# Kernel tuning notes

Hardware: AMD Instinct MI355X
Metric: run time of the kernel (lower is better)

Reference implementation:

```python
import jax, jax.numpy as jnp
import numpy as np

B, T, D = 4, 2048, 1024
NUM_HEADS = 16
HEAD_DIM = D // NUM_HEADS
MLP_HIDDEN = int(D * 4.0)  # 4096; gate_proj -> 2*MLP_HIDDEN
LN_EPS = 1e-6
GN_EPS = 1e-5


def rmsnorm(x, eps=1e-8):
    return x * jax.lax.rsqrt(jnp.mean(x * x, axis=-1, keepdims=True) + eps)


def bitlinear(x, w):
    # mmfreelm BitLinear: RMSNorm -> 8-bit per-token act quant (STE) -> ternary weight quant (STE)
    xn = rmsnorm(x)
    s = 127.0 / jnp.clip(jnp.max(jnp.abs(xn), axis=-1, keepdims=True), 1e-5, None)
    xq = xn + jax.lax.stop_gradient(jnp.clip(jnp.round(xn * s), -128, 127) / s - xn)
    ws = 1.0 / jnp.clip(jnp.mean(jnp.abs(w)), 1e-5, None)
    wq = w + jax.lax.stop_gradient(jnp.clip(jnp.round(w * ws), -1, 1) / ws - w)
    return xq @ wq.T


def layernorm(x, eps=LN_EPS):  # non-affine
    mu = jnp.mean(x, axis=-1, keepdims=True)
    var = jnp.mean((x - mu) ** 2, axis=-1, keepdims=True)
    return (x - mu) * jax.lax.rsqrt(var + eps)


def modulate(x, shift, scale):
    return x * (1.0 + scale[:, None, :]) + shift[:, None, :]


def hgrn_attention(x, wi, wf, wg, gnorm_w, wo):
    i = bitlinear(x, wi)
    f = jax.nn.sigmoid(bitlinear(x, wf))
    i = jax.nn.silu(i) * (1.0 - f)  # swiglu(i, 1-f)
    # gated linear recurrence h_t = f_t * h_{t-1} + i_t along time axis
    def combine(c1, c2):
        a1, b1 = c1
        a2, b2 = c2
        return a1 * a2, b1 * a2 + b2
    _, h = jax.lax.associative_scan(combine, (f, i), axis=1)
    g = bitlinear(x, wg)
    hh = h.reshape(B, T, NUM_HEADS, HEAD_DIM)
    gg = g.reshape(B, T, NUM_HEADS, HEAD_DIM)
    # FusedRMSNormSwishGate over head_dim
    o = rmsnorm(hh, GN_EPS) * gnorm_w * (gg * jax.nn.sigmoid(gg))
    return bitlinear(o.reshape(B, T, D), wo)


def hgrn_mlp(x, gate_w, down_w):
    y = bitlinear(x, gate_w)
    gate, y = jnp.split(y, 2, axis=-1)
    return bitlinear(jax.nn.silu(gate) * y, down_w)


def setup_inputs() -> dict:
    key = jax.random.key(0)
    ks = jax.random.split(key, 16)
    p = lambda k, shape: jax.random.normal(k, shape, dtype=jnp.float32) * 0.02
    return {
        "x": jax.random.normal(ks[0], (B, T, D), dtype=jnp.float32),
        "c": jax.random.normal(ks[1], (B, D), dtype=jnp.float32),
        "adaln_w": p(ks[2], (6 * D, D)),
        "adaln_b": jnp.zeros((6 * D,), dtype=jnp.float32),
        "wi": p(ks[3], (D, D)),
        "wf": p(ks[4], (D, D)),
        "wg": p(ks[5], (D, D)),
        "gnorm_w": jnp.ones((HEAD_DIM,), dtype=jnp.float32),
        "wo": p(ks[6], (D, D)),
        "gate_w": p(ks[7], (2 * MLP_HIDDEN, D)),
        "down_w": p(ks[8], (D, MLP_HIDDEN)),
    }


def reference(x, c, adaln_w, adaln_b, wi, wf, wg, gnorm_w, wo, gate_w, down_w):
    params = jax.nn.silu(c) @ adaln_w.T + adaln_b  # [B, 6D]
    (shift_msa, scale_msa, gate_msa,
     shift_mlp, scale_mlp, gate_mlp) = jnp.split(params, 6, axis=1)
    mod_x = modulate(layernorm(x), shift_msa, scale_msa)
    attn_out = hgrn_attention(mod_x, wi, wf, wg, gnorm_w, wo)
    x = x + gate_msa[:, None, :] * attn_out
    mlp_in = modulate(layernorm(x), shift_mlp, scale_mlp)
    x = x + gate_mlp[:, None, :] * hgrn_mlp(mlp_in, gate_w, down_w)
    return x
```

## Files before the change

kernel.cpp:

```cpp
#include <hip/hip_runtime.h>
#include <cstdint>
#include <cstddef>

#define B_   4
#define T_   2048
#define D_   1024
#define NTOK (B_*T_)
#define HID  4096
#define PDIM (6*D_)

typedef int v4i __attribute__((ext_vector_type(4)));

__device__ __forceinline__ float sigf(float x){ return 1.0f/(1.0f+expf(-x)); }

__device__ __forceinline__ float bsum256(float v, float* sm, int tid){
#pragma unroll
  for (int o=32;o;o>>=1) v += __shfl_down(v,o);
  if ((tid&63)==0) sm[tid>>6]=v;
  __syncthreads();
  float r = sm[0]+sm[1]+sm[2]+sm[3];
  __syncthreads();
  return r;
}
__device__ __forceinline__ void bsummax256(float& s, float& m, float* sm, int tid){
#pragma unroll
  for (int o=32;o;o>>=1){ s += __shfl_down(s,o); m = fmaxf(m,__shfl_down(m,o)); }
  if ((tid&63)==0){ sm[tid>>6]=s; sm[4+(tid>>6)]=m; }
  __syncthreads();
  s = sm[0]+sm[1]+sm[2]+sm[3];
  m = fmaxf(fmaxf(sm[4],sm[5]),fmaxf(sm[6],sm[7]));
  __syncthreads();
}

__device__ __forceinline__ uint32_t pack4(float a, float b, float c, float d, float k){
  int q0=(int)rintf(a*k); q0 = q0<-128?-128:(q0>127?127:q0);
  int q1=(int)rintf(b*k); q1 = q1<-128?-128:(q1>127?127:q1);
  int q2=(int)rintf(c*k); q2 = q2<-128?-128:(q2>127?127:q2);
  int q3=(int)rintf(d*k); q3 = q3<-128?-128:(q3>127?127:q3);
  return (uint32_t)(q0&255) | ((uint32_t)(q1&255)<<8) | ((uint32_t)(q2&255)<<16) | ((uint32_t)(q3&255)<<24);
}

struct WMeta {
  const float* w[6];
  int8_t* q[6];
  int n[6];
};

__global__ __launch_bounds__(256) void k_wabs(WMeta meta, float* __restrict__ partial){
  int mat = blockIdx.y;
  const float* w = meta.w[mat];
  int n = meta.n[mat];
  int tid = threadIdx.x;
  float s = 0.f;
  for (int i = blockIdx.x*256 + tid; i < n; i += 256*gridDim.x) s += fabsf(w[i]);
  __shared__ float sm[4];
#pragma unroll
  for (int o=32;o;o>>=1) s += __shfl_down(s,o);
  if ((tid&63)==0) sm[tid>>6]=s;
  __syncthreads();
  if (tid==0) partial[mat*256 + blockIdx.x] = sm[0]+sm[1]+sm[2]+sm[3];
}

__global__ __launch_bounds__(256) void k_wfin(WMeta meta, const float* __restrict__ partial, float* __restrict__ wdeq){
  int mat = blockIdx.x;
  int tid = threadIdx.x;
  float s = partial[mat*256 + tid];
  __shared__ float sm[4];
#pragma unroll
  for (int o=32;o;o>>=1) s += __shfl_down(s,o);
  if ((tid&63)==0) sm[tid>>6]=s;
  __syncthreads();
  if (tid==0){
    float mean = (sm[0]+sm[1]+sm[2]+sm[3]) / (float)meta.n[mat];
    wdeq[mat] = fmaxf(mean, 1e-5f);
  }
}

__global__ __launch_bounds__(256) void k_wquant(WMeta meta, const float* __restrict__ wdeq){
  int mat = blockIdx.y;
  const float* w = meta.w[mat];
  int8_t* q = meta.q[mat];
  int n = meta.n[mat];
  float ws = 1.0f / wdeq[mat];
  for (int i = blockIdx.x*256 + threadIdx.x; i < n; i += 256*gridDim.x){
    int v = (int)rintf(w[i]*ws);
    v = v < -1 ? -1 : (v > 1 ? 1 : v);
    q[i] = (int8_t)v;
  }
}

__global__ __launch_bounds__(256) void k_adaln(const float* __restrict__ c, const float* __restrict__ w,
                                               const float* __restrict__ bias, float* __restrict__ params){
  int wv = threadIdx.x>>6, lane = threadIdx.x&63;
  int oidx = blockIdx.x*4 + wv;
  int b = oidx / PDIM, j = oidx % PDIM;
  const float* cr = c + b*D_;
  const float* wr = w + (size_t)j*D_;
  float s = 0.f;
  for (int k = lane; k < D_; k += 64){
    float cv = cr[k];
    s += (cv*sigf(cv)) * wr[k];
  }
#pragma unroll
  for (int o=32;o;o>>=1) s += __shfl_down(s,o);
  if (lane==0) params[oidx] = s + bias[j];
}

template<int RES>
__global__ __launch_bounds__(256) void k_lnmodq(const float* __restrict__ xin,
    const float* __restrict__ addv, const float* __restrict__ params,
    int shift_off, int scale_off, int gate_off,
    float* __restrict__ x2out, int8_t* __restrict__ xq, float* __restrict__ dq){
  int tok = blockIdx.x;
  int b = tok >> 11;
  int tid = threadIdx.x;
  __shared__ float sm[8];
  const float* pb = params + (size_t)b*PDIM;
  float4 v = ((const float4*)(xin + (size_t)tok*D_))[tid];
  if (RES){
    float4 a = ((const float4*)(addv + (size_t)tok*D_))[tid];
    float4 g = ((const float4*)(pb + gate_off))[tid];
    v.x = fmaf(g.x,a.x,v.x); v.y = fmaf(g.y,a.y,v.y);
    v.z = fmaf(g.z,a.z,v.z); v.w = fmaf(g.w,a.w,v.w);
    ((float4*)(x2out + (size_t)tok*D_))[tid] = v;
  }
  float mu = bsum256(v.x+v.y+v.z+v.w, sm, tid) * (1.0f/D_);
  float t0=v.x-mu, t1=v.y-mu, t2=v.z-mu, t3=v.w-mu;
  float var = bsum256(t0*t0+t1*t1+t2*t2+t3*t3, sm, tid) * (1.0f/D_);
  float rstd = rsqrtf(var + 1e-6f);
  float4 sc = ((const float4*)(pb + scale_off))[tid];
  float4 sh = ((const float4*)(pb + shift_off))[tid];
  float y0 = fmaf(t0*rstd, 1.0f+sc.x, sh.x);
  float y1 = fmaf(t1*rstd, 1.0f+sc.y, sh.y);
  float y2 = fmaf(t2*rstd, 1.0f+sc.z, sh.z);
  float y3 = fmaf(t3*rstd, 1.0f+sc.w, sh.w);
  float ssq = y0*y0+y1*y1+y2*y2+y3*y3;
  float mx = fmaxf(fmaxf(fabsf(y0),fabsf(y1)),fmaxf(fabsf(y2),fabsf(y3)));
  bsummax256(ssq, mx, sm, tid);
  float rms = rsqrtf(ssq*(1.0f/D_) + 1e-8f);
  float a = fmaxf(mx*rms, 1e-5f);
  float s = 127.0f/a;
  float k = rms*s;
  ((uint32_t*)(xq + (size_t)tok*D_))[tid] = pack4(y0,y1,y2,y3,k);
  if (tid==0) dq[tok] = 1.0f/s;
}

template<int FINAL>
__global__ __launch_bounds__(256) void k_gemm(const int8_t* __restrict__ Aq, const int8_t* __restrict__ Bq,
    float* __restrict__ Out, const float* __restrict__ adq, const float* __restrict__ wdq_ptr,
    int N, int K, const float* __restrict__ resid, const float* __restrict__ params){
  __shared__ int8_t lA[8192], lB[8192];
  const int tid = threadIdx.x;
  const int wave = tid>>6, lane = tid&63;
  const int row0 = blockIdx.y<<7, col0 = blockIdx.x<<7;
  const int wm = (wave>>1)<<6, wn = (wave&1)<<6;
  v4i acc[4][4];
#pragma unroll
  for (int m=0;m<4;m++)
#pragma unroll
    for (int n=0;n<4;n++) acc[m][n] = (v4i){0,0,0,0};
  const int rA = lane&15, kg = lane>>4;
  for (int k0=0;k0<K;k0+=64){
#pragma unroll
    for (int p=0;p<2;p++){
      int idx = p*256 + tid;
      int r = idx>>2, cb = (idx&3)<<4;
      const int8_t* ga = Aq + (size_t)(row0+r)*K + k0 + cb;
      const int8_t* gb = Bq + (size_t)(col0+r)*K + k0 + cb;
      __builtin_amdgcn_global_load_lds((const __attribute__((address_space(1))) void*)ga,
        (__attribute__((address_space(3))) void*)(lA + p*4096 + wave*1024), 16, 0, 0);
      __builtin_amdgcn_global_load_lds((const __attribute__((address_space(1))) void*)gb,
        (__attribute__((address_space(3))) void*)(lB + p*4096 + wave*1024), 16, 0, 0);
    }
    __syncthreads();
    const v4i* la4 = (const v4i*)lA;
    const v4i* lb4 = (const v4i*)lB;
    v4i af[4], bf[4];
#pragma unroll
    for (int m=0;m<4;m++) af[m] = la4[((wm + m*16 + rA)<<2) + kg];
#pragma unroll
    for (int n=0;n<4;n++) bf[n] = lb4[((wn + n*16 + rA)<<2) + kg];
#pragma unroll
    for (int m=0;m<4;m++)
#pragma unroll
      for (int n=0;n<4;n++)
        acc[m][n] = __builtin_amdgcn_mfma_i32_16x16x64_i8(af[m], bf[n], acc[m][n], 0, 0, 0);
    __syncthreads();
  }
  float wdq = wdq_ptr[0];
  int rr = (lane>>4)<<2, cl = lane&15;
#pragma unroll
  for (int m=0;m<4;m++){
#pragma unroll
    for (int r=0;r<4;r++){
      int row = row0 + wm + m*16 + rr + r;
      float scale = adq[row]*wdq;
#pragma unroll
      for (int n=0;n<4;n++){
        int col = col0 + wn + n*16 + cl;
        size_t oi = (size_t)row*N + col;
        float val = (float)acc[m][n][r]*scale;
        if (FINAL){
          int bb = row>>11;
          val = resid[oi] + params[(size_t)bb*PDIM + 5*D_ + col]*val;
        }
        Out[oi] = val;
      }
    }
  }
}

__global__ __launch_bounds__(256) void k_gemm_gate(const int8_t* __restrict__ Aq, const int8_t* __restrict__ Wg,
    float* __restrict__ Out, const float* __restrict__ adq, const float* __restrict__ wdq_ptr, int K){
  __shared__ int8_t lA[8192], lBg[8192], lBy[8192];
  const int tid = threadIdx.x;
  const int wave = tid>>6, lane = tid&63;
  const int row0 = blockIdx.y<<7, col0 = blockIdx.x<<7;
  const int wm = (wave>>1)<<6, wn = (wave&1)<<6;
  v4i accg[4][4], accy[4][4];
#pragma unroll
  for (int m=0;m<4;m++)
#pragma unroll
    for (int n=0;n<4;n++){ accg[m][n] = (v4i){0,0,0,0}; accy[m][n] = (v4i){0,0,0,0}; }
  const int rA = lane&15, kg = lane>>4;
  for (int k0=0;k0<K;k0+=64){
#pragma unroll
    for (int p=0;p<2;p++){
      int idx = p*256 + tid;
      int r = idx>>2, cb = (idx&3)<<4;
      const int8_t* ga  = Aq + (size_t)(row0+r)*K + k0 + cb;
      const int8_t* gbg = Wg + (size_t)(col0+r)*K + k0 + cb;
      const int8_t* gby = Wg + (size_t)(HID + col0+r)*K + k0 + cb;
      __builtin_amdgcn_global_load_lds((const __attribute__((address_space(1))) void*)ga,
        (__attribute__((address_space(3))) void*)(lA  + p*4096 + wave*1024), 16, 0, 0);
      __builtin_amdgcn_global_load_lds((const __attribute__((address_space(1))) void*)gbg,
        (__attribute__((address_space(3))) void*)(lBg + p*4096 + wave*1024), 16, 0, 0);
      __builtin_amdgcn_global_load_lds((const __attribute__((address_space(1))) void*)gby,
        (__attribute__((address_space(3))) void*)(lBy + p*4096 + wave*1024), 16, 0, 0);
    }
    __syncthreads();
    const v4i* la4 = (const v4i*)lA;
    const v4i* lg4 = (const v4i*)lBg;
    const v4i* ly4 = (const v4i*)lBy;
    v4i af[4], bg[4], by[4];
#pragma unroll
    for (int m=0;m<4;m++) af[m] = la4[((wm + m*16 + rA)<<2) + kg];
#pragma unroll
    for (int n=0;n<4;n++){ bg[n] = lg4[((wn + n*16 + rA)<<2) + kg]; by[n] = ly4[((wn + n*16 + rA)<<2) + kg]; }
#pragma unroll
    for (int m=0;m<4;m++)
#pragma unroll
      for (int n=0;n<4;n++){
        accg[m][n] = __builtin_amdgcn_mfma_i32_16x16x64_i8(af[m], bg[n], accg[m][n], 0, 0, 0);
        accy[m][n] = __builtin_amdgcn_mfma_i32_16x16x64_i8(af[m], by[n], accy[m][n], 0, 0, 0);
      }
    __syncthreads();
  }
  float wdq = wdq_ptr[0];
  int rr = (lane>>4)<<2, cl = lane&15;
#pragma unroll
  for (int m=0;m<4;m++){
#pragma unroll
    for (int r=0;r<4;r++){
      int row = row0 + wm + m*16 + rr + r;
      float scale = adq[row]*wdq;
#pragma unroll
      for (int n=0;n<4;n++){
        int col = col0 + wn + n*16 + cl;
        float gv = (float)accg[m][n][r]*scale;
        float yv = (float)accy[m][n][r]*scale;
        Out[(size_t)row*HID + col] = gv*sigf(gv)*yv;
      }
    }
  }
}

__global__ __launch_bounds__(256) void k_ewif(float* __restrict__ ibuf, float* __restrict__ fbuf, int n4){
  for (int k = blockIdx.x*256 + threadIdx.x; k < n4; k += gridDim.x*256){
    float4 iv = ((float4*)ibuf)[k];
    float4 fv = ((float4*)fbuf)[k];
    float f0=sigf(fv.x), f1=sigf(fv.y), f2=sigf(fv.z), f3=sigf(fv.w);
    float4 io, fo;
    io.x = iv.x*sigf(iv.x)*(1.0f-f0);
    io.y = iv.y*sigf(iv.y)*(1.0f-f1);
    io.z = iv.z*sigf(iv.z)*(1.0f-f2);
    io.w = iv.w*sigf(iv.w)*(1.0f-f3);
    fo.x=f0; fo.y=f1; fo.z=f2; fo.w=f3;
    ((float4*)ibuf)[k] = io;
    ((float4*)fbuf)[k] = fo;
  }
}

__global__ __launch_bounds__(256) void k_scanA(const float* __restrict__ f, const float* __restrict__ ii,
                                               float* __restrict__ Ac, float* __restrict__ Hc){
  int idx = blockIdx.x*256 + threadIdx.x;
  int ch = idx >> 12;
  int c  = idx & 4095;
  int b = c >> 10, d = c & 1023;
  size_t base = ((size_t)(b*T_ + ch*64))*D_ + d;
  float a = 1.f, h = 0.f;
  for (int t=0;t<64;t++){
    float ft = f[base + (size_t)t*D_];
    float it = ii[base + (size_t)t*D_];
    a *= ft;
    h = ft*h + it;
  }
  Ac[ch*4096 + c] = a;
  Hc[ch*4096 + c] = h;
}
__global__ __launch_bounds__(256) void k_scanB(const float* __restrict__ Ac, const float* __restrict__ Hc,
                                               float* __restrict__ H0){
  int c = blockIdx.x*256 + threadIdx.x;
  float h = 0.f;
  for (int ch=0; ch<32; ch++){
    H0[ch*4096 + c] = h;
    h = Ac[ch*4096 + c]*h + Hc[ch*4096 + c];
  }
}
__global__ __launch_bounds__(256) void k_scanC(const float* __restrict__ f, const float* __restrict__ ii,
                                               const float* __restrict__ H0, float* __restrict__ hout){
  int idx = blockIdx.x*256 + threadIdx.x;
  int ch = idx >> 12;
  int c  = idx & 4095;
  int b = c >> 10, d = c & 1023;
  size_t base = ((size_t)(b*T_ + ch*64))*D_ + d;
  float h = H0[ch*4096 + c];
  for (int t=0;t<64;t++){
    float ft = f[base + (size_t)t*D_];
    float it = ii[base + (size_t)t*D_];
    h = ft*h + it;
    hout[base + (size_t)t*D_] = h;
  }
}

__global__ __launch_bounds__(256) void k_ogateq(const float* __restrict__ h, const float* __restrict__ g,
    const float* __restrict__ gnw, int8_t* __restrict__ xq, float* __restrict__ dq){
  int tok = blockIdx.x, tid = threadIdx.x;
  __shared__ float sm[8];
  float4 hv = ((const float4*)(h + (size_t)tok*D_))[tid];
  float ss = hv.x*hv.x + hv.y*hv.y + hv.z*hv.z + hv.w*hv.w;
  ss += __shfl_xor(ss,1); ss += __shfl_xor(ss,2); ss += __shfl_xor(ss,4); ss += __shfl_xor(ss,8);
  float rh = rsqrtf(ss*(1.0f/64.0f) + 1e-5f);
  float4 gv = ((const float4*)(g + (size_t)tok*D_))[tid];
  int hd = (tid*4)&63;
  float o0 = hv.x*rh*gnw[hd+0]*(gv.x*sigf(gv.x));
  float o1 = hv.y*rh*gnw[hd+1]*(gv.y*sigf(gv.y));
  float o2 = hv.z*rh*gnw[hd+2]*(gv.z*sigf(gv.z));
  float o3 = hv.w*rh*gnw[hd+3]*(gv.w*sigf(gv.w));
  float ssq = o0*o0+o1*o1+o2*o2+o3*o3;
  float mx = fmaxf(fmaxf(fabsf(o0),fabsf(o1)),fmaxf(fabsf(o2),fabsf(o3)));
  bsummax256(ssq, mx, sm, tid);
  float rms = rsqrtf(ssq*(1.0f/D_) + 1e-8f);
  float a = fmaxf(mx*rms, 1e-5f);
  float s = 127.0f/a;
  float k = rms*s;
  ((uint32_t*)(xq + (size_t)tok*D_))[tid] = pack4(o0,o1,o2,o3,k);
  if (tid==0) dq[tok] = 1.0f/s;
}

__global__ __launch_bounds__(256) void k_mlpq(const float* __restrict__ hsw, int8_t* __restrict__ xq,
                                              float* __restrict__ dq){
  int tok = blockIdx.x, tid = threadIdx.x;
  __shared__ float sm[8];
  const float4* r4 = (const float4*)(hsw + (size_t)tok*HID);
  float4 v[4];
  float ssq = 0.f, mx = 0.f;
#pragma unroll
  for (int j=0;j<4;j++){
    v[j] = r4[tid + j*256];
    ssq += v[j].x*v[j].x + v[j].y*v[j].y + v[j].z*v[j].z + v[j].w*v[j].w;
    mx = fmaxf(mx, fmaxf(fmaxf(fabsf(v[j].x),fabsf(v[j].y)),fmaxf(fabsf(v[j].z),fabsf(v[j].w))));
  }
  bsummax256(ssq, mx, sm, tid);
  float rms = rsqrtf(ssq*(1.0f/HID) + 1e-8f);
  float a = fmaxf(mx*rms, 1e-5f);
  float s = 127.0f/a;
  float k = rms*s;
#pragma unroll
  for (int j=0;j<4;j++)
    ((uint32_t*)(xq + (size_t)tok*HID))[tid + j*256] = pack4(v[j].x,v[j].y,v[j].z,v[j].w,k);
  if (tid==0) dq[tok] = 1.0f/s;
}


extern "C" void kernel_launch(void* const* d_in, const int* in_sizes, int n_in,
                              void* d_out, int out_size, void* d_ws, size_t ws_size,
                              hipStream_t stream){
  (void)in_sizes; (void)n_in; (void)out_size; (void)ws_size;
  const float* x     = (const float*)d_in[0];
  const float* c     = (const float*)d_in[1];
  const float* aw    = (const float*)d_in[2];
  const float* ab    = (const float*)d_in[3];
  const float* wi    = (const float*)d_in[4];
  const float* wf    = (const float*)d_in[5];
  const float* wg    = (const float*)d_in[6];
  const float* gnw   = (const float*)d_in[7];
  const float* wo    = (const float*)d_in[8];
  const float* wgate = (const float*)d_in[9];
  const float* wdown = (const float*)d_in[10];
  float* out = (float*)d_out;

  char* ws = (char*)d_ws;
  size_t off = 0;
  auto alloc = [&](size_t b){ size_t r = off; off += (b + 255) & ~(size_t)255; return r; };

  size_t oWQ[6];
  oWQ[0] = alloc(1024*1024);
  oWQ[1] = alloc(1024*1024);
  oWQ[2] = alloc(1024*1024);
  oWQ[3] = alloc(1024*1024);
  oWQ[4] = alloc((size_t)8192*1024);
  oWQ[5] = alloc((size_t)1024*4096);
  size_t oWDEQ = alloc(6*4);
  size_t oPART = alloc(6*256*4);
  size_t oPAR  = alloc((size_t)4*PDIM*4);
  size_t oS1 = alloc(NTOK*4), oS2 = alloc(NTOK*4), oS3 = alloc(NTOK*4), oSH = alloc(NTOK*4);
  size_t oXQA  = alloc((size_t)NTOK*D_);
  size_t oPOOL = alloc((size_t)5*NTOK*D_*4);
  size_t oX2   = alloc((size_t)NTOK*D_*4);
  size_t oSA = alloc((size_t)32*4096*4), oSHc = alloc((size_t)32*4096*4), oSH0 = alloc((size_t)32*4096*4);

  float*  params = (float*)(ws+oPAR);
  float*  wdeq   = (float*)(ws+oWDEQ);
  float*  part   = (float*)(ws+oPART);
  float*  s1 = (float*)(ws+oS1); float* s2 = (float*)(ws+oS2);
  float*  s3 = (float*)(ws+oS3); float* sh = (float*)(ws+oSH);
  int8_t* xqa = (int8_t*)(ws+oXQA);
  float*  bufI  = (float*)(ws+oPOOL);
  float*  bufF  = bufI + (size_t)NTOK*D_;
  float*  bufG  = bufF + (size_t)NTOK*D_;
  float*  bufH  = bufG + (size_t)NTOK*D_;
  float*  bufAT = bufH + (size_t)NTOK*D_;
  float*  hsw   = bufI;
  int8_t* xqh   = (int8_t*)bufAT;
  float*  x2    = (float*)(ws+oX2);
  float*  scAc = (float*)(ws+oSA); float* scHc = (float*)(ws+oSHc); float* scH0 = (float*)(ws+oSH0);

  WMeta meta;
  meta.w[0]=wi; meta.w[1]=wf; meta.w[2]=wg; meta.w[3]=wo; meta.w[4]=wgate; meta.w[5]=wdown;
  for (int m=0;m<6;m++) meta.q[m] = (int8_t*)(ws+oWQ[m]);
  meta.n[0]=meta.n[1]=meta.n[2]=meta.n[3]=1024*1024; meta.n[4]=8192*1024; meta.n[5]=1024*4096;

  k_wabs  <<<dim3(256,6), 256, 0, stream>>>(meta, part);
  k_wfin  <<<6,           256, 0, stream>>>(meta, part, wdeq);
  k_wquant<<<dim3(2048,6),256, 0, stream>>>(meta, wdeq);

  k_adaln<<<PDIM, 256, 0, stream>>>(c, aw, ab, params);

  k_lnmodq<0><<<NTOK, 256, 0, stream>>>(x, nullptr, params, 0, D_, 0, nullptr, xqa, s1);
  k_gemm<0><<<dim3(8,64), 256, 0, stream>>>(xqa, meta.q[0], bufI, s1, wdeq+0, D_, D_, nullptr, nullptr);
  k_gemm<0><<<dim3(8,64), 256, 0, stream>>>(xqa, meta.q[1], bufF, s1, wdeq+1, D_, D_, nullptr, nullptr);
  k_gemm<0><<<dim3(8,64), 256, 0, stream>>>(xqa, meta.q[2], bufG, s1, wdeq+2, D_, D_, nullptr, nullptr);
  k_ewif<<<2048, 256, 0, stream>>>(bufI, bufF, NTOK*D_/4);
  k_scanA<<<512, 256, 0, stream>>>(bufF, bufI, scAc, scHc);
  k_scanB<<<16,  256, 0, stream>>>(scAc, scHc, scH0);
  k_scanC<<<512, 256, 0, stream>>>(bufF, bufI, scH0, bufH);
  k_ogateq<<<NTOK, 256, 0, stream>>>(bufH, bufG, gnw, xqa, s2);
  k_gemm<0><<<dim3(8,64), 256, 0, stream>>>(xqa, meta.q[3], bufAT, s2, wdeq+3, D_, D_, nullptr, nullptr);

  k_lnmodq<1><<<NTOK, 256, 0, stream>>>(x, bufAT, params, 3*D_, 4*D_, 2*D_, x2, xqa, s3);
  k_gemm_gate<<<dim3(32,64), 256, 0, stream>>>(xqa, meta.q[4], hsw, s3, wdeq+4, D_);
  k_mlpq<<<NTOK, 256, 0, stream>>>(hsw, xqh, sh);
  k_gemm<1><<<dim3(8,64), 256, 0, stream>>>(xqh, meta.q[5], out, sh, wdeq+5, D_, HID, x2, params);
}
```

Measured before the change: 703.5 us.

## Double-buffer GEMMs, swizzle LDS, fuse i/f gemms with gating, store bf16 intermediates

Several ideas land together. The int8 GEMMs get double-buffered LDS staging, and an XOR swizzle on the k-word layout is applied when quantizing weights and activations so LDS reads avoid bank conflicts. The wi and wf GEMMs are fused into one kernel whose epilogue applies sigmoid and swiglu, which removes the separate elementwise pass. The i, f, g and MLP hidden intermediates are stored as bf16 instead of fp32 to cut memory traffic. The bf16 storage lowers the precision of values fed into the scan and requantization, and the doubled LDS use may reduce occupancy.

```diff
diff --git a/kernel.cpp b/kernel.cpp
--- a/kernel.cpp
+++ b/kernel.cpp
@@ -10,8 +10,20 @@
 #define PDIM (6*D_)
 
 typedef int v4i __attribute__((ext_vector_type(4)));
+typedef __attribute__((ext_vector_type(8))) unsigned short ushort8v;
 
 __device__ __forceinline__ float sigf(float x){ return 1.0f/(1.0f+expf(-x)); }
+
+__device__ __forceinline__ float b2f(uint16_t u){ union{uint32_t i; float f;} x; x.i = ((uint32_t)u)<<16; return x.f; }
+__device__ __forceinline__ uint16_t f2b(float f){
+  union{float f; uint32_t i;} x; x.f=f;
+  uint32_t r = x.i + 0x7fff + ((x.i>>16)&1);
+  return (uint16_t)(r>>16);
+}
+
+__device__ __forceinline__ int swz_word(int wi, int row){
+  return (wi & ~15) | ((((wi>>2)&3) ^ ((row>>1)&3))<<2) | (wi&3);
+}
 
 __device__ __forceinline__ float bsum256(float v, float* sm, int tid){
 #pragma unroll
@@ -44,6 +56,7 @@
   const float* w[6];
   int8_t* q[6];
   int n[6];
+  int kws[6];
 };
 
 __global__ __launch_bounds__(256) void k_wabs(WMeta meta, float* __restrict__ partial){
@@ -79,13 +92,20 @@
 __global__ __launch_bounds__(256) void k_wquant(WMeta meta, const float* __restrict__ wdeq){
   int mat = blockIdx.y;
   const float* w = meta.w[mat];
-  int8_t* q = meta.q[mat];
-  int n = meta.n[mat];
+  uint32_t* q = (uint32_t*)meta.q[mat];
+  int nw = meta.n[mat]>>2;
+  int kws = meta.kws[mat];
+  int kwmask = (1<<kws)-1;
   float ws = 1.0f / wdeq[mat];
-  for (int i = blockIdx.x*256 + threadIdx.x; i < n; i += 256*gridDim.x){
-    int v = (int)rintf(w[i]*ws);
-    v = v < -1 ? -1 : (v > 1 ? 1 : v);
-    q[i] = (int8_t)v;
+  for (int i = blockIdx.x*256 + threadIdx.x; i < nw; i += 256*gridDim.x){
+    float4 v = ((const float4*)w)[i];
+    int q0=(int)rintf(v.x*ws); q0=q0<-1?-1:(q0>1?1:q0);
+    int q1=(int)rintf(v.y*ws); q1=q1<-1?-1:(q1>1?1:q1);
+    int q2=(int)rintf(v.z*ws); q2=q2<-1?-1:(q2>1?1:q2);
+    int q3=(int)rintf(v.w*ws); q3=q3<-1?-1:(q3>1?1:q3);
+    uint32_t packed = (uint32_t)(q0&255) | ((uint32_t)(q1&255)<<8) | ((uint32_t)(q2&255)<<16) | ((uint32_t)(q3&255)<<24);
+    int row = i >> kws, wi = i & kwmask;
+    q[((size_t)row<<kws) + swz_word(wi,row)] = packed;
   }
 }
 
@@ -141,15 +161,15 @@
   float a = fmaxf(mx*rms, 1e-5f);
   float s = 127.0f/a;
   float k = rms*s;
-  ((uint32_t*)(xq + (size_t)tok*D_))[tid] = pack4(y0,y1,y2,y3,k);
+  ((uint32_t*)(xq + (size_t)tok*D_))[swz_word(tid,tok)] = pack4(y0,y1,y2,y3,k);
   if (tid==0) dq[tok] = 1.0f/s;
 }
 
-template<int FINAL>
+template<int MODE>
 __global__ __launch_bounds__(256) void k_gemm(const int8_t* __restrict__ Aq, const int8_t* __restrict__ Bq,
-    float* __restrict__ Out, const float* __restrict__ adq, const float* __restrict__ wdq_ptr,
+    void* __restrict__ Outv, const float* __restrict__ adq, const float* __restrict__ wdq_ptr,
     int N, int K, const float* __restrict__ resid, const float* __restrict__ params){
-  __shared__ int8_t lA[8192], lB[8192];
+  __shared__ int8_t lA[2][8192], lB[2][8192];
   const int tid = threadIdx.x;
   const int wave = tid>>6, lane = tid&63;
   const int row0 = blockIdx.y<<7, col0 = blockIdx.x<<7;
@@ -160,33 +180,45 @@
 #pragma unroll
     for (int n=0;n<4;n++) acc[m][n] = (v4i){0,0,0,0};
   const int rA = lane&15, kg = lane>>4;
-  for (int k0=0;k0<K;k0+=64){
+  const int axor = (rA>>1)&3;
+  const int r_st = tid>>2, cb_st = (tid&3)<<4;
+
+  auto STAGE = [&](int buf, int k0){
 #pragma unroll
     for (int p=0;p<2;p++){
-      int idx = p*256 + tid;
-      int r = idx>>2, cb = (idx&3)<<4;
-      const int8_t* ga = Aq + (size_t)(row0+r)*K + k0 + cb;
-      const int8_t* gb = Bq + (size_t)(col0+r)*K + k0 + cb;
-      __builtin_amdgcn_global_load_lds((const __attribute__((address_space(1))) void*)ga,
-        (__attribute__((address_space(3))) void*)(lA + p*4096 + wave*1024), 16, 0, 0);
-      __builtin_amdgcn_global_load_lds((const __attribute__((address_space(1))) void*)gb,
-        (__attribute__((address_space(3))) void*)(lB + p*4096 + wave*1024), 16, 0, 0);
+      int r = p*64 + r_st;
+      __builtin_amdgcn_global_load_lds((const __attribute__((address_space(1))) void*)(Aq + (size_t)(row0+r)*K + k0 + cb_st),
+        (__attribute__((address_space(3))) void*)(&lA[buf][p*4096 + wave*1024]), 16, 0, 0);
+      __builtin_amdgcn_global_load_lds((const __attribute__((address_space(1))) void*)(Bq + (size_t)(col0+r)*K + k0 + cb_st),
+        (__attribute__((address_space(3))) void*)(&lB[buf][p*4096 + wave*1024]), 16, 0, 0);
     }
-    __syncthreads();
-    const v4i* la4 = (const v4i*)lA;
-    const v4i* lb4 = (const v4i*)lB;
+  };
+  auto COMPUTE = [&](int buf){
+    const v4i* la4 = (const v4i*)lA[buf];
+    const v4i* lb4 = (const v4i*)lB[buf];
     v4i af[4], bf[4];
 #pragma unroll
-    for (int m=0;m<4;m++) af[m] = la4[((wm + m*16 + rA)<<2) + kg];
-#pragma unroll
-    for (int n=0;n<4;n++) bf[n] = lb4[((wn + n*16 + rA)<<2) + kg];
+    for (int m=0;m<4;m++){ int r = wm + m*16 + rA; af[m] = la4[(r<<2) + (kg^axor)]; }
+#pragma unroll
+    for (int n=0;n<4;n++){ int r = wn + n*16 + rA; bf[n] = lb4[(r<<2) + (kg^axor)]; }
 #pragma unroll
     for (int m=0;m<4;m++)
 #pragma unroll
       for (int n=0;n<4;n++)
         acc[m][n] = __builtin_amdgcn_mfma_i32_16x16x64_i8(af[m], bf[n], acc[m][n], 0, 0, 0);
+  };
+
+  STAGE(0, 0);
+  __syncthreads();
+  int cur = 0;
+  for (int k0=64; k0<K; k0+=64){
+    STAGE(cur^1, k0);
+    COMPUTE(cur);
     __syncthreads();
-  }
+    cur ^= 1;
+  }
+  COMPUTE(cur);
+
   float wdq = wdq_ptr[0];
   int rr = (lane>>4)<<2, cl = lane&15;
 #pragma unroll
@@ -200,98 +232,103 @@
         int col = col0 + wn + n*16 + cl;
         size_t oi = (size_t)row*N + col;
         float val = (float)acc[m][n][r]*scale;
-        if (FINAL){
+        if (MODE==0) ((float*)Outv)[oi] = val;
+        if (MODE==1) ((uint16_t*)Outv)[oi] = f2b(val);
+        if (MODE==2){
           int bb = row>>11;
-          val = resid[oi] + params[(size_t)bb*PDIM + 5*D_ + col]*val;
+          ((float*)Outv)[oi] = resid[oi] + params[(size_t)bb*PDIM + 5*D_ + col]*val;
         }
-        Out[oi] = val;
       }
     }
   }
 }
 
-__global__ __launch_bounds__(256) void k_gemm_gate(const int8_t* __restrict__ Aq, const int8_t* __restrict__ Wg,
-    float* __restrict__ Out, const float* __restrict__ adq, const float* __restrict__ wdq_ptr, int K){
-  __shared__ int8_t lA[8192], lBg[8192], lBy[8192];
+template<int MODE>
+__global__ __launch_bounds__(256) void k_gemm2(const int8_t* __restrict__ Aq, const int8_t* __restrict__ Bq0,
+    const int8_t* __restrict__ Bq1, uint16_t* __restrict__ out0, uint16_t* __restrict__ out1,
+    const float* __restrict__ adq, const float* __restrict__ wdq_ptr, int i0, int i1, int N, int K){
+  __shared__ int8_t lA[2][8192], lB0[2][8192], lB1[2][8192];
   const int tid = threadIdx.x;
   const int wave = tid>>6, lane = tid&63;
   const int row0 = blockIdx.y<<7, col0 = blockIdx.x<<7;
   const int wm = (wave>>1)<<6, wn = (wave&1)<<6;
-  v4i accg[4][4], accy[4][4];
+  v4i acc0[4][4], acc1[4][4];
 #pragma unroll
   for (int m=0;m<4;m++)
 #pragma unroll
-    for (int n=0;n<4;n++){ accg[m][n] = (v4i){0,0,0,0}; accy[m][n] = (v4i){0,0,0,0}; }
+    for (int n=0;n<4;n++){ acc0[m][n] = (v4i){0,0,0,0}; acc1[m][n] = (v4i){0,0,0,0}; }
   const int rA = lane&15, kg = lane>>4;
-  for (int k0=0;k0<K;k0+=64){
+  const int axor = (rA>>1)&3;
+  const int r_st = tid>>2, cb_st = (tid&3)<<4;
+
+  auto STAGE = [&](int buf, int k0){
 #pragma unroll
     for (int p=0;p<2;p++){
-      int idx = p*256 + tid;
-      int r = idx>>2, cb = (idx&3)<<4;
-      const int8_t* ga  = Aq + (size_t)(row0+r)*K + k0 + cb;
-      const int8_t* gbg = Wg + (size_t)(col0+r)*K + k0 + cb;
-      const int8_t* gby = Wg + (size_t)(HID + col0+r)*K + k0 + cb;
-      __builtin_amdgcn_global_load_lds((const __attribute__((address_space(1))) void*)ga,
-        (__attribute__((address_space(3))) void*)(lA  + p*4096 + wave*1024), 16, 0, 0);
-      __builtin_amdgcn_global_load_lds((const __attribute__((address_space(1))) void*)gbg,
-        (__attribute__((address_space(3))) void*)(lBg + p*4096 + wave*1024), 16, 0, 0);
-      __builtin_amdgcn_global_load_lds((const __attribute__((address_space(1))) void*)gby,
-        (__attribute__((address_space(3))) void*)(lBy + p*4096 + wave*1024), 16, 0, 0);
+      int r = p*64 + r_st;
+      __builtin_amdgcn_global_load_lds((const __attribute__((address_space(1))) void*)(Aq  + (size_t)(row0+r)*K + k0 + cb_st),
+        (__attribute__((address_space(3))) void*)(&lA[buf][p*4096 + wave*1024]), 16, 0, 0);
+      __builtin_amdgcn_global_load_lds((const __attribute__((address_space(1))) void*)(Bq0 + (size_t)(col0+r)*K + k0 + cb_st),
+        (__attribute__((address_space(3))) void*)(&lB0[buf][p*4096 + wave*1024]), 16, 0, 0);
+      __builtin_amdgcn_global_load_lds((const __attribute__((address_space(1))) void*)(Bq1 + (size_t)(col0+r)*K + k0 + cb_st),
+        (__attribute__((address_space(3))) void*)(&lB1[buf][p*4096 + wave*1024]), 16, 0, 0);
     }
+  };
+  auto COMPUTE = [&](int buf){
+    const v4i* la4 = (const v4i*)lA[buf];
+    const v4i* lb4 = (const v4i*)lB0[buf];
+    const v4i* lc4 = (const v4i*)lB1[buf];
+    v4i af[4], bf[4], cf[4];
+#pragma unroll
+    for (int m=0;m<4;m++){ int r = wm + m*16 + rA; af[m] = la4[(r<<2) + (kg^axor)]; }
+#pragma unroll
+    for (int n=0;n<4;n++){ int r = wn + n*16 + rA; bf[n] = lb4[(r<<2) + (kg^axor)]; cf[n] = lc4[(r<<2) + (kg^axor)]; }
+#pragma unroll
+    for (int m=0;m<4;m++)
+#pragma unroll
+      for (int n=0;n<4;n++){
+        acc0[m][n] = __builtin_amdgcn_mfma_i32_16x16x64_i8(af[m], bf[n], acc0[m][n], 0, 0, 0);
+        acc1[m][n] = __builtin_amdgcn_mfma_i32_16x16x64_i8(af[m], cf[n], acc1[m][n], 0, 0, 0);
+      }
+  };
+
+  STAGE(0, 0);
+  __syncthreads();
+  int cur = 0;
+  for (int k0=64; k0<K; k0+=64){
+    STAGE(cur^1, k0);
+    COMPUTE(cur);
     __syncthreads();
-    const v4i* la4 = (const v4i*)lA;
-    const v4i* lg4 = (const v4i*)lBg;
-    const v4i* ly4 = (const v4i*)lBy;
-    v4i af[4], bg[4], by[4];
-#pragma unroll
-    for (int m=0;m<4;m++) af[m] = la4[((wm + m*16 + rA)<<2) + kg];
-#pragma unroll
-    for (int n=0;n<4;n++){ bg[n] = lg4[((wn + n*16 + rA)<<2) + kg]; by[n] = ly4[((wn + n*16 + rA)<<2) + kg]; }
-#pragma unroll
-    for (int m=0;m<4;m++)
-#pragma unroll
-      for (int n=0;n<4;n++){
-        accg[m][n] = __builtin_amdgcn_mfma_i32_16x16x64_i8(af[m], bg[n], accg[m][n], 0, 0, 0);
-        accy[m][n] = __builtin_amdgcn_mfma_i32_16x16x64_i8(af[m], by[n], accy[m][n], 0, 0, 0);
-      }
-    __syncthreads();
-  }
-  float wdq = wdq_ptr[0];
+    cur ^= 1;
+  }
+  COMPUTE(cur);
+
+  float wdq0 = wdq_ptr[i0], wdq1 = wdq_ptr[i1];
   int rr = (lane>>4)<<2, cl = lane&15;
 #pragma unroll
   for (int m=0;m<4;m++){
 #pragma unroll
     for (int r=0;r<4;r++){
       int row = row0 + wm + m*16 + rr + r;
-      float scale = adq[row]*wdq;
+      float scale = adq[row];
 #pragma unroll
       for (int n=0;n<4;n++){
         int col = col0 + wn + n*16 + cl;
-        float gv = (float)accg[m][n][r]*scale;
-        float yv = (float)accy[m][n][r]*scale;
-        Out[(size_t)row*HID + col] = gv*sigf(gv)*yv;
+        size_t oi = (size_t)row*N + col;
+        float v0 = (float)acc0[m][n][r]*scale*wdq0;
+        float v1 = (float)acc1[m][n][r]*scale*wdq1;
+        if (MODE==0){
+          float fs = sigf(v1);
+          out0[oi] = f2b(v0*sigf(v0)*(1.0f-fs));
+          out1[oi] = f2b(fs);
+        } else {
+          out0[oi] = f2b(v0*sigf(v0)*v1);
+        }
       }
     }
   }
 }
 
-__global__ __launch_bounds__(256) void k_ewif(float* __restrict__ ibuf, float* __restrict__ fbuf, int n4){
-  for (int k = blockIdx.x*256 + threadIdx.x; k < n4; k += gridDim.x*256){
-    float4 iv = ((float4*)ibuf)[k];
-    float4 fv = ((float4*)fbuf)[k];
-    float f0=sigf(fv.x), f1=sigf(fv.y), f2=sigf(fv.z), f3=sigf(fv.w);
-    float4 io, fo;
-    io.x = iv.x*sigf(iv.x)*(1.0f-f0);
-    io.y = iv.y*sigf(iv.y)*(1.0f-f1);
-    io.z = iv.z*sigf(iv.z)*(1.0f-f2);
-    io.w = iv.w*sigf(iv.w)*(1.0f-f3);
-    fo.x=f0; fo.y=f1; fo.z=f2; fo.w=f3;
-    ((float4*)ibuf)[k] = io;
-    ((float4*)fbuf)[k] = fo;
-  }
-}
-
-__global__ __launch_bounds__(256) void k_scanA(const float* __restrict__ f, const float* __restrict__ ii,
+__global__ __launch_bounds__(256) void k_scanA(const uint16_t* __restrict__ f, const uint16_t* __restrict__ ii,
                                                float* __restrict__ Ac, float* __restrict__ Hc){
   int idx = blockIdx.x*256 + threadIdx.x;
   int ch = idx >> 12;
@@ -300,8 +337,8 @@
   size_t base = ((size_t)(b*T_ + ch*64))*D_ + d;
   float a = 1.f, h = 0.f;
   for (int t=0;t<64;t++){
-    float ft = f[base + (size_t)t*D_];
-    float it = ii[base + (size_t)t*D_];
+    float ft = b2f(f[base + (size_t)t*D_]);
+    float it = b2f(ii[base + (size_t)t*D_]);
     a *= ft;
     h = ft*h + it;
   }
@@ -317,7 +354,7 @@
     h = Ac[ch*4096 + c]*h + Hc[ch*4096 + c];
   }
 }
-__global__ __launch_bounds__(256) void k_scanC(const float* __restrict__ f, const float* __restrict__ ii,
+__global__ __launch_bounds__(256) void k_scanC(const uint16_t* __restrict__ f, const uint16_t* __restrict__ ii,
                                                const float* __restrict__ H0, float* __restrict__ hout){
   int idx = blockIdx.x*256 + threadIdx.x;
   int ch = idx >> 12;
@@ -326,14 +363,14 @@
   size_t base = ((size_t)(b*T_ + ch*64))*D_ + d;
   float h = H0[ch*4096 + c];
   for (int t=0;t<64;t++){
-    float ft = f[base + (size_t)t*D_];
-    float it = ii[base + (size_t)t*D_];
+    float ft = b2f(f[base + (size_t)t*D_]);
+    float it = b2f(ii[base + (size_t)t*D_]);
     h = ft*h + it;
     hout[base + (size_t)t*D_] = h;
   }
 }
 
-__global__ __launch_bounds__(256) void k_ogateq(const float* __restrict__ h, const float* __restrict__ g,
+__global__ __launch_bounds__(256) void k_ogateq(const float* __restrict__ h, const uint16_t* __restrict__ g,
     const float* __restrict__ gnw, int8_t* __restrict__ xq, float* __restrict__ dq){
   int tok = blockIdx.x, tid = threadIdx.x;
   __shared__ float sm[8];
@@ -341,12 +378,13 @@
   float ss = hv.x*hv.x + hv.y*hv.y + hv.z*hv.z + hv.w*hv.w;
   ss += __shfl_xor(ss,1); ss += __shfl_xor(ss,2); ss += __shfl_xor(ss,4); ss += __shfl_xor(ss,8);
   float rh = rsqrtf(ss*(1.0f/64.0f) + 1e-5f);
-  float4 gv = ((const float4*)(g + (size_t)tok*D_))[tid];
+  ushort4 gv = ((const ushort4*)(g + (size_t)tok*D_))[tid];
+  float g0=b2f(gv.x), g1=b2f(gv.y), g2=b2f(gv.z), g3=b2f(gv.w);
   int hd = (tid*4)&63;
-  float o0 = hv.x*rh*gnw[hd+0]*(gv.x*sigf(gv.x));
-  float o1 = hv.y*rh*gnw[hd+1]*(gv.y*sigf(gv.y));
-  float o2 = hv.z*rh*gnw[hd+2]*(gv.z*sigf(gv.z));
-  float o3 = hv.w*rh*gnw[hd+3]*(gv.w*sigf(gv.w));
+  float o0 = hv.x*rh*gnw[hd+0]*(g0*sigf(g0));
+  float o1 = hv.y*rh*gnw[hd+1]*(g1*sigf(g1));
+  float o2 = hv.z*rh*gnw[hd+2]*(g2*sigf(g2));
+  float o3 = hv.w*rh*gnw[hd+3]*(g3*sigf(g3));
   float ssq = o0*o0+o1*o1+o2*o2+o3*o3;
   float mx = fmaxf(fmaxf(fabsf(o0),fabsf(o1)),fmaxf(fabsf(o2),fabsf(o3)));
   bsummax256(ssq, mx, sm, tid);
@@ -354,31 +392,40 @@
   float a = fmaxf(mx*rms, 1e-5f);
   float s = 127.0f/a;
   float k = rms*s;
-  ((uint32_t*)(xq + (size_t)tok*D_))[tid] = pack4(o0,o1,o2,o3,k);
+  ((uint32_t*)(xq + (size_t)tok*D_))[swz_word(tid,tok)] = pack4(o0,o1,o2,o3,k);
   if (tid==0) dq[tok] = 1.0f/s;
 }
 
-__global__ __launch_bounds__(256) void k_mlpq(const float* __restrict__ hsw, int8_t* __restrict__ xq,
+__global__ __launch_bounds__(256) void k_mlpq(const uint16_t* __restrict__ hsw, int8_t* __restrict__ xq,
                                               float* __restrict__ dq){
   int tok = blockIdx.x, tid = threadIdx.x;
   __shared__ float sm[8];
-  const float4* r4 = (const float4*)(hsw + (size_t)tok*HID);
-  float4 v[4];
+  const ushort8v* r8 = (const ushort8v*)(hsw + (size_t)tok*HID);
+  float v[2][8];
   float ssq = 0.f, mx = 0.f;
 #pragma unroll
-  for (int j=0;j<4;j++){
-    v[j] = r4[tid + j*256];
-    ssq += v[j].x*v[j].x + v[j].y*v[j].y + v[j].z*v[j].z + v[j].w*v[j].w;
-    mx = fmaxf(mx, fmaxf(fmaxf(fabsf(v[j].x),fabsf(v[j].y)),fmaxf(fabsf(v[j].z),fabsf(v[j].w))));
+  for (int j=0;j<2;j++){
+    ushort8v u = r8[tid + j*256];
+#pragma unroll
+    for (int e=0;e<8;e++){
+      float fv = b2f(u[e]);
+      v[j][e] = fv;
+      ssq += fv*fv;
+      mx = fmaxf(mx, fabsf(fv));
+    }
   }
   bsummax256(ssq, mx, sm, tid);
   float rms = rsqrtf(ssq*(1.0f/HID) + 1e-8f);
   float a = fmaxf(mx*rms, 1e-5f);
   float s = 127.0f/a;
   float k = rms*s;
-#pragma unroll
-  for (int j=0;j<4;j++)
-    ((uint32_t*)(xq + (size_t)tok*HID))[tid + j*256] = pack4(v[j].x,v[j].y,v[j].z,v[j].w,k);
+  uint32_t* qw = (uint32_t*)(xq + (size_t)tok*HID);
+#pragma unroll
+  for (int j=0;j<2;j++){
+    int u = tid + j*256;
+    qw[swz_word(2*u,   tok)] = pack4(v[j][0],v[j][1],v[j][2],v[j][3],k);
+    qw[swz_word(2*u+1, tok)] = pack4(v[j][4],v[j][5],v[j][6],v[j][7],k);
+  }
   if (tid==0) dq[tok] = 1.0f/s;
 }
 
@@ -416,7 +463,7 @@
   size_t oPAR  = alloc((size_t)4*PDIM*4);
   size_t oS1 = alloc(NTOK*4), oS2 = alloc(NTOK*4), oS3 = alloc(NTOK*4), oSH = alloc(NTOK*4);
   size_t oXQA  = alloc((size_t)NTOK*D_);
-  size_t oPOOL = alloc((size_t)5*NTOK*D_*4);
+  size_t oPOOL = alloc((size_t)3*NTOK*D_*2 + (size_t)2*NTOK*D_*4);
   size_t oX2   = alloc((size_t)NTOK*D_*4);
   size_t oSA = alloc((size_t)32*4096*4), oSHc = alloc((size_t)32*4096*4), oSH0 = alloc((size_t)32*4096*4);
 
@@ -426,13 +473,13 @@
   float*  s1 = (float*)(ws+oS1); float* s2 = (float*)(ws+oS2);
   float*  s3 = (float*)(ws+oS3); float* sh = (float*)(ws+oSH);
   int8_t* xqa = (int8_t*)(ws+oXQA);
-  float*  bufI  = (float*)(ws+oPOOL);
-  float*  bufF  = bufI + (size_t)NTOK*D_;
-  float*  bufG  = bufF + (size_t)NTOK*D_;
-  float*  bufH  = bufG + (size_t)NTOK*D_;
-  float*  bufAT = bufH + (size_t)NTOK*D_;
-  float*  hsw   = bufI;
-  int8_t* xqh   = (int8_t*)bufAT;
+  uint16_t* bI  = (uint16_t*)(ws+oPOOL);
+  uint16_t* bF  = bI + (size_t)NTOK*D_;
+  uint16_t* bG  = bF + (size_t)NTOK*D_;
+  float*    bufH  = (float*)(bG + (size_t)NTOK*D_);
+  float*    bufAT = bufH + (size_t)NTOK*D_;
+  uint16_t* hsw   = bI;
+  int8_t*   xqh   = (int8_t*)bufAT;
   float*  x2    = (float*)(ws+oX2);
   float*  scAc = (float*)(ws+oSA); float* scHc = (float*)(ws+oSHc); float* scH0 = (float*)(ws+oSH0);
 
@@ -440,26 +487,25 @@
   meta.w[0]=wi; meta.w[1]=wf; meta.w[2]=wg; meta.w[3]=wo; meta.w[4]=wgate; meta.w[5]=wdown;
   for (int m=0;m<6;m++) meta.q[m] = (int8_t*)(ws+oWQ[m]);
   meta.n[0]=meta.n[1]=meta.n[2]=meta.n[3]=1024*1024; meta.n[4]=8192*1024; meta.n[5]=1024*4096;
+  meta.kws[0]=meta.kws[1]=meta.kws[2]=meta.kws[3]=meta.kws[4]=8; meta.kws[5]=10;
 
   k_wabs  <<<dim3(256,6), 256, 0, stream>>>(meta, part);
   k_wfin  <<<6,           256, 0, stream>>>(meta, part, wdeq);
-  k_wquant<<<dim3(2048,6),256, 0, stream>>>(meta, wdeq);
+  k_wquant<<<dim3(1024,6),256, 0, stream>>>(meta, wdeq);
 
   k_adaln<<<PDIM, 256, 0, stream>>>(c, aw, ab, params);
 
   k_lnmodq<0><<<NTOK, 256, 0, stream>>>(x, nullptr, params, 0, D_, 0, nullptr, xqa, s1);
-  k_gemm<0><<<dim3(8,64), 256, 0, stream>>>(xqa, meta.q[0], bufI, s1, wdeq+0, D_, D_, nullptr, nullptr);
-  k_gemm<0><<<dim3(8,64), 256, 0, stream>>>(xqa, meta.q[1], bufF, s1, wdeq+1, D_, D_, nullptr, nullptr);
-  k_gemm<0><<<dim3(8,64), 256, 0, stream>>>(xqa, meta.q[2], bufG, s1, wdeq+2, D_, D_, nullptr, nullptr);
-  k_ewif<<<2048, 256, 0, stream>>>(bufI, bufF, NTOK*D_/4);
-  k_scanA<<<512, 256, 0, stream>>>(bufF, bufI, scAc, scHc);
+  k_gemm2<0><<<dim3(8,64), 256, 0, stream>>>(xqa, meta.q[0], meta.q[1], bI, bF, s1, wdeq, 0, 1, D_, D_);
+  k_gemm<1><<<dim3(8,64), 256, 0, stream>>>(xqa, meta.q[2], bG, s1, wdeq+2, D_, D_, nullptr, nullptr);
+  k_scanA<<<512, 256, 0, stream>>>(bF, bI, scAc, scHc);
   k_scanB<<<16,  256, 0, stream>>>(scAc, scHc, scH0);
-  k_scanC<<<512, 256, 0, stream>>>(bufF, bufI, scH0, bufH);
-  k_ogateq<<<NTOK, 256, 0, stream>>>(bufH, bufG, gnw, xqa, s2);
+  k_scanC<<<512, 256, 0, stream>>>(bF, bI, scH0, bufH);
+  k_ogateq<<<NTOK, 256, 0, stream>>>(bufH, bG, gnw, xqa, s2);
   k_gemm<0><<<dim3(8,64), 256, 0, stream>>>(xqa, meta.q[3], bufAT, s2, wdeq+3, D_, D_, nullptr, nullptr);
 
   k_lnmodq<1><<<NTOK, 256, 0, stream>>>(x, bufAT, params, 3*D_, 4*D_, 2*D_, x2, xqa, s3);
-  k_gemm_gate<<<dim3(32,64), 256, 0, stream>>>(xqa, meta.q[4], hsw, s3, wdeq+4, D_);
+  k_gemm2<1><<<dim3(32,64), 256, 0, stream>>>(xqa, meta.q[4], meta.q[4] + (size_t)HID*1024, hsw, nullptr, s3, wdeq+4, 0, 0, HID, D_);
   k_mlpq<<<NTOK, 256, 0, stream>>>(hsw, xqh, sh);
-  k_gemm<1><<<dim3(8,64), 256, 0, stream>>>(xqh, meta.q[5], out, sh, wdeq+5, D_, HID, x2, params);
-}
+  k_gemm<2><<<dim3(8,64), 256, 0, stream>>>(xqh, meta.q[5], out, sh, wdeq+5, D_, HID, x2, params);
+}
```

After: 603.9 us. 14.2% less time.
